# Kernel tuning notes

Hardware: AMD Instinct MI355X
Metric: run time of the kernel (lower is better)

## Reference

```python
import jax, jax.numpy as jnp
import numpy as np

# Dimensions: B batches, E links, T time steps, F flows, rank-r factors, K unrolled iters
B, E, T, F = 16, 256, 4096, 512
RANK = 10
NUM_ITER = 5


def setup_inputs() -> dict:
    key = jax.random.key(0)
    ks = jax.random.split(key, 9)
    Y = jax.random.normal(ks[0], (B, E, T), dtype=jnp.float32)
    R = (jax.random.uniform(ks[1], (B, E, F)) < 0.1).astype(jnp.float32)
    Omega = (jax.random.uniform(ks[2], (B, E, T)) < 0.9).astype(jnp.float32)
    P0 = jax.random.normal(ks[3], (B, E, RANK), dtype=jnp.float32) * 0.1
    Q0 = jax.random.normal(ks[4], (B, T, RANK), dtype=jnp.float32) * 0.1
    # per-iteration learned log-parameters of the unrolled network
    lam_log = jax.random.normal(ks[5], (NUM_ITER,), dtype=jnp.float32) * 0.1 - 1.0
    mu_log = jax.random.normal(ks[6], (NUM_ITER,), dtype=jnp.float32) * 0.1 - 1.0
    nu_log = jax.random.normal(ks[7], (NUM_ITER,), dtype=jnp.float32) * 0.1
    gamma_logit = jax.random.normal(ks[8], (NUM_ITER,), dtype=jnp.float32) * 0.1
    return {"Y": Y, "R": R, "Omega": Omega, "P0": P0, "Q0": Q0,
            "lam_log": lam_log, "mu_log": mu_log, "nu_log": nu_log,
            "gamma_logit": gamma_logit}


def reference(Y, R, Omega, P0, Q0, lam_log, mu_log, nu_log, gamma_logit):
    """Unrolled BSCA: Y ~ X + R @ A + noise on observed entries (Omega mask),
    X relaxed low-rank via factors P (B,E,r), Q (B,T,r); A sparse anomalies (B,F,T).
    Each iteration: rank-r ridge solves for P and Q (left=False -> rhs @ inv(lhs)),
    relaxed X update, soft-thresholded BSCA direction for A + convex-combination step."""
    rank = P0.shape[-1]
    eye = jnp.eye(rank, dtype=Y.dtype)
    X = Omega * Y                     # (B,E,T) init relaxed variable
    A = jnp.zeros((*Y.shape[:-2], R.shape[-1], Y.shape[-1]), dtype=Y.dtype)  # (B,F,T)
    P, Q = P0, Q0
    A_scale = (R * R).mT @ (Omega * Omega)          # (B,F,T)
    noobs = A_scale == 0
    A_scale_safe = A_scale + noobs.astype(Y.dtype)
    for k in range(NUM_ITER):
        lam = jnp.exp(lam_log[k])
        mu = jnp.exp(mu_log[k])
        nu = jnp.exp(nu_log[k])
        gamma = jax.nn.sigmoid(gamma_logit[k])
        regp = lam / nu
        # P update: P = (X @ Q) @ inv(Q^T Q + regp I)   (right solve; lhs symmetric)
        lhsQ = Q.mT @ Q + regp * eye                 # (B,r,r)
        P = jnp.linalg.solve(lhsQ, (X @ Q).mT).mT    # (B,E,r)
        # Q update: Q = (X^T @ P) @ inv(P^T P + regp I)
        lhsP = P.mT @ P + regp * eye
        Q = jnp.linalg.solve(lhsP, (X.mT @ P).mT).mT # (B,T,r)
        # X update (relaxed): X = (Omega*err + nu*P Q^T) / (Omega^2 + nu)
        RA = R @ A                                   # (B,E,T)
        err = Omega * (Y - RA)
        X = (Omega * err + nu * (P @ Q.mT)) / (Omega * Omega + nu)
        # A update: soft-thresholded best-response + convex combination step
        resid = Omega * (Y - X - RA)                 # (B,E,T)
        BA = A + (R.mT @ resid) / A_scale_safe       # (B,F,T)
        A_dir = jnp.sign(BA) * jnp.maximum(jnp.abs(BA) - mu / A_scale_safe, 0.0)
        A_dir = jnp.where(noobs, 0.0, A_dir)
        A = A + gamma * (A_dir - A)
    return A
```

## Files before the change

### kernel.cpp

```cpp
#include <hip/hip_runtime.h>
#include <stdint.h>

#define BB 16
#define EE 256
#define TT 4096
#define FF 512
#define RK 10
#define NIT 5

typedef short bf16x8 __attribute__((ext_vector_type(8)));
typedef float f32x4  __attribute__((ext_vector_type(4)));

__device__ __forceinline__ unsigned short f2bf(float x){
  unsigned int u = __float_as_uint(x);
  unsigned int r = (u + 0x7FFFu + ((u >> 16) & 1u)) >> 16;
  return (unsigned short)r;
}
__device__ __forceinline__ float bf2f(unsigned short s){
  return __uint_as_float(((unsigned int)s) << 16);
}

__device__ __forceinline__ void gld16(const void* g, void* l){
  __builtin_amdgcn_global_load_lds((const __attribute__((address_space(1))) unsigned int*)g,
                                   (__attribute__((address_space(3))) unsigned int*)l,
                                   16, 0, 0);
}

__device__ __forceinline__ int ssw(int r, int s){
  return ((s ^ (r & 3) ^ ((r >> 2) & 3)) << 3);
}


__global__ void k_params(const float* lam_log, const float* mu_log,
                         const float* nu_log, const float* gl, float* prm){
  int k = threadIdx.x;
  if (k < NIT){
    float lam = expf(lam_log[k]);
    float mu  = expf(mu_log[k]);
    float nu  = expf(nu_log[k]);
    float gam = 1.0f/(1.0f+expf(-gl[k]));
    prm[k*8+0]=lam; prm[k*8+1]=mu; prm[k*8+2]=nu; prm[k*8+3]=gam; prm[k*8+4]=lam/nu;
  }
}

__global__ void k_initX(const float4* __restrict__ Y, const float4* __restrict__ Om,
                        float4* __restrict__ X, ushort4* __restrict__ Omb){
  int i = blockIdx.x*256 + threadIdx.x;
  float4 y = Y[i], o = Om[i];
  X[i] = make_float4(y.x*o.x, y.y*o.y, y.z*o.z, y.w*o.w);
  ushort4 ob; ob.x=f2bf(o.x); ob.y=f2bf(o.y); ob.z=f2bf(o.z); ob.w=f2bf(o.w);
  Omb[i] = ob;
}

__global__ void k_ombit(const float* __restrict__ Om, unsigned int* __restrict__ Ombit){
  int tid = threadIdx.x;
  int wv = tid >> 6, lane = tid & 63;
  size_t base = (size_t)blockIdx.x*8192 + (size_t)wv*2048;
  for (int it=0; it<32; ++it){
    float om = Om[base + it*64 + lane];
    unsigned long long m = __ballot(om != 0.0f);
    if (lane==0)  Ombit[(base>>5) + it*2]     = (unsigned int)m;
    if (lane==32) Ombit[(base>>5) + it*2 + 1] = (unsigned int)(m>>32);
  }
}

__global__ void k_qtrans(const float* __restrict__ Q0, float* __restrict__ Qt){
  int idx = blockIdx.x*256 + threadIdx.x;
  int b = idx >> 12, t = idx & (TT-1);
  #pragma unroll
  for (int j=0;j<RK;j++)
    Qt[((size_t)b*RK + j)*TT + t] = Q0[(size_t)idx*RK + j];
}

__global__ void k_rbf(const float4* __restrict__ R, ushort4* __restrict__ Rb){
  int i = blockIdx.x*256 + threadIdx.x;
  float4 v = R[i];
  ushort4 o; o.x=f2bf(v.x); o.y=f2bf(v.y); o.z=f2bf(v.z); o.w=f2bf(v.w);
  Rb[i] = o;
}

__global__ void k_rtransb(const float* __restrict__ Rm, unsigned short* __restrict__ Rbt){
  int f = blockIdx.x, b = blockIdx.y, e = threadIdx.x;
  Rbt[((size_t)b*FF + f)*EE + e] = f2bf(Rm[((size_t)b*EE + e)*FF + f]);
}

__global__ void k_omtrans(const unsigned short* __restrict__ Omb,
                          unsigned short* __restrict__ OmbT){
  __shared__ unsigned short sT[64][66];
  int b  = blockIdx.z;
  int E0 = blockIdx.y*64, T0 = blockIdx.x*64;
  int tid = threadIdx.x;
  int fi = tid >> 4;
  int m  = tid & 15;
  #pragma unroll
  for (int pass=0; pass<4; ++pass){
    int e = pass*16 + fi;
    ushort4 v = *(const ushort4*)(Omb + ((size_t)(b*EE + E0 + e))*TT + T0 + m*4);
    sT[e][m*4+0]=v.x; sT[e][m*4+1]=v.y; sT[e][m*4+2]=v.z; sT[e][m*4+3]=v.w;
  }
  __syncthreads();
  #pragma unroll
  for (int pass=0; pass<4; ++pass){
    int t  = pass*16 + fi;
    int e4 = m*4;
    ushort4 o;
    o.x = sT[e4+0][t]; o.y = sT[e4+1][t];
    o.z = sT[e4+2][t]; o.w = sT[e4+3][t];
    *(ushort4*)(OmbT + ((size_t)b*TT + T0 + t)*EE + E0 + e4) = o;
  }
}


__global__ void k_lhsQ(const float* __restrict__ Qt, const float* __restrict__ prm,
                       float* __restrict__ lhs, int k){
  int p = blockIdx.x, b = blockIdx.y;
  int i = 0, rem = p;
  while (rem >= i+1){ rem -= (i+1); ++i; }
  int j = rem;
  const float* qi = Qt + ((size_t)b*RK + i)*TT;
  const float* qj = Qt + ((size_t)b*RK + j)*TT;
  float a = 0.0f;
  for (int t = threadIdx.x*4; t < TT; t += 1024){
    float4 x = *(const float4*)(qi+t);
    float4 y = *(const float4*)(qj+t);
    a += x.x*y.x + x.y*y.y + x.z*y.z + x.w*y.w;
  }
  __shared__ float red[256];
  red[threadIdx.x] = a; __syncthreads();
  for (int s=128; s>0; s>>=1){
    if (threadIdx.x < s) red[threadIdx.x] += red[threadIdx.x+s];
    __syncthreads();
  }
  if (threadIdx.x==0){
    float v = red[0];
    if (i==j) v += prm[k*8+4];
    lhs[(b*RK+i)*RK + j] = v;
    lhs[(b*RK+j)*RK + i] = v;
  }
}

__global__ void k_lhsP(const float* __restrict__ P, const float* __restrict__ prm,
                       float* __restrict__ lhs, int k){
  int p = blockIdx.x, b = blockIdx.y;
  int i = 0, rem = p;
  while (rem >= i+1){ rem -= (i+1); ++i; }
  int j = rem;
  int e = threadIdx.x;
  const float* pr = P + ((size_t)b*EE + e)*RK;
  float a = pr[i]*pr[j];
  __shared__ float red[256];
  red[threadIdx.x] = a; __syncthreads();
  for (int s=128; s>0; s>>=1){
    if (threadIdx.x < s) red[threadIdx.x] += red[threadIdx.x+s];
    __syncthreads();
  }
  if (threadIdx.x==0){
    float v = red[0];
    if (i==j) v += prm[k*8+4];
    lhs[(b*RK+i)*RK + j] = v;
    lhs[(b*RK+j)*RK + i] = v;
  }
}

__global__ void k_invert(const float* __restrict__ lhs, float* __restrict__ inv){
  int b = blockIdx.x;
  __shared__ float aug[RK][2*RK];
  int tid = threadIdx.x;
  int i = tid / (2*RK), j = tid % (2*RK);
  bool act = tid < RK*2*RK;
  if (act) aug[i][j] = (j < RK) ? lhs[(b*RK+i)*RK + j] : ((j-RK)==i ? 1.0f : 0.0f);
  __syncthreads();
  for (int kk=0; kk<RK; ++kk){
    float pinv = 1.0f / aug[kk][kk];
    __syncthreads();
    if (act && i==kk) aug[i][j] *= pinv;
    __syncthreads();
    float factor = (act && i!=kk) ? aug[i][kk] : 0.0f;
    float pivrow = act ? aug[kk][j] : 0.0f;
    __syncthreads();
    if (act && i!=kk) aug[i][j] -= factor * pivrow;
    __syncthreads();
  }
  if (act && j >= RK) inv[(b*RK+i)*RK + (j-RK)] = aug[i][j];
}

__global__ void k_Pupd(const float* __restrict__ X, const float* __restrict__ Qt,
                       const float* __restrict__ inv, float* __restrict__ P){
  int e = blockIdx.x, b = blockIdx.y;
  const float* xr = X + ((size_t)b*EE + e)*TT;
  const float* qb = Qt + (size_t)b*RK*TT;
  float acc[RK];
  #pragma unroll
  for (int j=0;j<RK;j++) acc[j]=0.0f;
  for (int t = threadIdx.x*4; t < TT; t += 1024){
    float4 x = *(const float4*)(xr+t);
    #pragma unroll
    for (int j=0;j<RK;j++){
      float4 q = *(const float4*)(qb + (size_t)j*TT + t);
      acc[j] += x.x*q.x + x.y*q.y + x.z*q.z + x.w*q.w;
    }
  }
  __shared__ float partial[4][RK];
  int lane = threadIdx.x & 63, wv = threadIdx.x >> 6;
  #pragma unroll
  for (int j=0;j<RK;j++){
    float v = acc[j];
    for (int s=32;s>0;s>>=1) v += __shfl_down(v, s, 64);
    if (lane==0) partial[wv][j] = v;
  }
  __syncthreads();
  if (threadIdx.x < RK){
    int i = threadIdx.x;
    float out = 0.0f;
    #pragma unroll
    for (int j=0;j<RK;j++){
      float xq = partial[0][j]+partial[1][j]+partial[2][j]+partial[3][j];
      out += xq * inv[(b*RK+j)*RK + i];
    }
    P[((size_t)b*EE + e)*RK + i] = out;
  }
}

__global__ void k_Qupd(const float* __restrict__ X, const float* __restrict__ P,
                       const float* __restrict__ inv, float* __restrict__ Qt){
  int b = blockIdx.y;
  int t = blockIdx.x*256 + threadIdx.x;
  __shared__ float sP[EE*RK];
  __shared__ float sInv[RK*RK];
  for (int i=threadIdx.x; i<EE*RK; i+=256) sP[i] = P[(size_t)b*EE*RK + i];
  if (threadIdx.x < RK*RK) sInv[threadIdx.x] = inv[b*RK*RK + threadIdx.x];
  __syncthreads();
  float acc[RK];
  #pragma unroll
  for (int j=0;j<RK;j++) acc[j]=0.0f;
  const float* xb = X + (size_t)b*EE*TT + t;
  for (int e=0;e<EE;e++){
    float x = xb[(size_t)e*TT];
    #pragma unroll
    for (int j=0;j<RK;j++) acc[j] += x * sP[e*RK+j];
  }
  #pragma unroll
  for (int i=0;i<RK;i++){
    float q = 0.0f;
    #pragma unroll
    for (int j=0;j<RK;j++) q += acc[j]*sInv[j*RK+i];
    Qt[((size_t)b*RK + i)*TT + t] = q;
  }
}

__global__ __launch_bounds__(256) void k_gemm1m(
    const unsigned short* __restrict__ Abt, const unsigned short* __restrict__ Rb,
    const float* __restrict__ Y, const unsigned int* __restrict__ Ombit,
    const float* __restrict__ Qt, const float* __restrict__ P,
    const float* __restrict__ prm, float* __restrict__ X,
    unsigned short* __restrict__ residT, int k)
{
  __shared__ __align__(16) unsigned char lds[20480];
  int id = blockIdx.x;
  int b  = id >> 7;
  int e0 = ((id >> 6) & 1) * 128;
  int t0 = (id & 63) * 64;
  int tid  = threadIdx.x;
  int lane = tid & 63, wid = tid >> 6;
  int lr = lane & 15, lg = lane >> 4;
  int wm = wid >> 1, wn = wid & 1;

  f32x4 acc[2][4];
  #pragma unroll
  for (int m=0;m<2;++m)
    #pragma unroll
    for (int n=0;n<4;++n)
      #pragma unroll
      for (int i=0;i<4;++i) acc[m][n][i]=0.0f;

  if (k > 0){
    int swz  = ((lg ^ (lr & 3) ^ ((lr >> 2) & 3)) << 4);
    int aoff = (wm*32 + lr)*64 + swz;
    int boff = 4096 + (wn*64 + lr)*64 + swz;
    int rA = tid >> 2, sA = tid & 3;
    int c0 = tid, c1 = tid + 256;
    int rB0 = c0 >> 2, sB0 = c0 & 3;
    int rB1 = c1 >> 2, sB1 = c1 & 3;
    const unsigned short* gA  = Abt + ((size_t)b*TT + t0 + rA)*FF + ssw(rA,sA);
    const unsigned short* gB0 = Rb  + ((size_t)(b*EE + e0 + rB0))*FF + ssw(rB0,sB0);
    const unsigned short* gB1 = Rb  + ((size_t)(b*EE + e0 + rB1))*FF + ssw(rB1,sB1);
    unsigned char* lA  = lds + tid*16;
    unsigned char* lB0 = lds + 4096 + c0*16;
    unsigned char* lB1 = lds + 4096 + c1*16;

    for (int kk=0; kk<16; ++kk){
      __syncthreads();
      int f0k = kk*32;
      gld16(gA  + f0k, lA);
      gld16(gB0 + f0k, lB0);
      gld16(gB1 + f0k, lB1);
      asm volatile("s_waitcnt vmcnt(0)" ::: "memory");
      __syncthreads();
      bf16x8 af[2], bb[4];
      #pragma unroll
      for (int m=0;m<2;++m) af[m] = *(const bf16x8*)(lds + aoff + m*1024);
      #pragma unroll
      for (int n=0;n<4;++n) bb[n] = *(const bf16x8*)(lds + boff + n*1024);
      #pragma unroll
      for (int m=0;m<2;++m)
        #pragma unroll
        for (int n=0;n<4;++n)
          acc[m][n] = __builtin_amdgcn_mfma_f32_16x16x32_bf16(af[m], bb[n], acc[m][n], 0, 0, 0);
    }
  }

  __syncthreads();
  unsigned short* wbuf = (unsigned short*)(lds + wid*2176);
  float* Pl = (float*)(lds + 12288);
  float* Ql = (float*)(lds + 12288 + 5120);
  for (int idx = tid; idx < 128*RK; idx += 256)
    Pl[idx] = P[((size_t)(b*EE + e0))*RK + idx];
  for (int idx = tid; idx < RK*64; idx += 256){
    int j = idx >> 6, t = idx & 63;
    Ql[idx] = Qt[((size_t)(b*RK + j))*TT + t0 + t];
  }
  __syncthreads();

  float nu = prm[k*8+2];
  #pragma unroll
  for (int m=0;m<2;++m){
    int tq = wm*32 + m*16 + lg*4;
    float4 ql4[RK];
    #pragma unroll
    for (int j=0;j<RK;++j) ql4[j] = *(const float4*)(Ql + j*64 + tq);
    asm volatile("" ::: "memory");
    #pragma unroll
    for (int n=0;n<4;++n){
      int eloc = wn*64 + n*16 + lr;
      const float* pr = Pl + eloc*RK;
      float4 pq = {0,0,0,0};
      #pragma unroll
      for (int j=0;j<RK;++j){
        float pj = pr[j];
        pq.x += pj*ql4[j].x; pq.y += pj*ql4[j].y;
        pq.z += pj*ql4[j].z; pq.w += pj*ql4[j].w;
      }
      f32x4 ra = acc[m][n];
      size_t off = ((size_t)(b*EE + e0 + eloc))*TT + t0 + tq;
      float4 y = *(const float4*)(Y + off);
      unsigned int w = Ombit[off >> 5];
      int sh = (int)(off & 31);
      float4 xo; float rs0, rs1, rs2, rs3;
      {
        float om2 = (w>>(sh+0))&1 ? 1.0f : 0.0f; float d = y.x - ra[0];
        xo.x = (om2*d + nu*pq.x)/(om2 + nu); rs0 = om2*(y.x - xo.x - ra[0]);
      }{
        float om2 = (w>>(sh+1))&1 ? 1.0f : 0.0f; float d = y.y - ra[1];
        xo.y = (om2*d + nu*pq.y)/(om2 + nu); rs1 = om2*(y.y - xo.y - ra[1]);
      }{
        float om2 = (w>>(sh+2))&1 ? 1.0f : 0.0f; float d = y.z - ra[2];
        xo.z = (om2*d + nu*pq.z)/(om2 + nu); rs2 = om2*(y.z - xo.z - ra[2]);
      }{
        float om2 = (w>>(sh+3))&1 ? 1.0f : 0.0f; float d = y.w - ra[3];
        xo.w = (om2*d + nu*pq.w)/(om2 + nu); rs3 = om2*(y.w - xo.w - ra[3]);
      }
      *(float4*)(X + off) = xo;
      int wc = n*16 + lr;
      wbuf[(lg*4+0)*68 + wc] = f2bf(rs0);
      wbuf[(lg*4+1)*68 + wc] = f2bf(rs1);
      wbuf[(lg*4+2)*68 + wc] = f2bf(rs2);
      wbuf[(lg*4+3)*68 + wc] = f2bf(rs3);
    }
    asm volatile("" ::: "memory");
    #pragma unroll
    for (int j2=0;j2<4;++j2){
      int row = j2*4 + lg;
      int c4  = lr*4;
      ushort4 vv = *(const ushort4*)(wbuf + row*68 + c4);
      *(ushort4*)(residT + ((size_t)b*TT + t0 + wm*32 + m*16 + row)*EE + e0 + wn*64 + c4) = vv;
    }
    asm volatile("" ::: "memory");
  }
}

__device__ __forceinline__ float aupd(float a, float g, unsigned short asu,
                                      float mu, float gamma){
  float as = bf2f(asu);
  bool no = (as == 0.0f);
  float rs = 1.0f / (no ? 1.0f : as);
  float ba = a + g*rs;
  float ad = copysignf(fmaxf(fabsf(ba) - mu*rs, 0.0f), ba);
  if (no) ad = 0.0f;
  return a + gamma*(ad - a);
}

__global__ __launch_bounds__(256) void k_gemm2m(
    const unsigned short* __restrict__ residT, const unsigned short* __restrict__ Rbt,
    const unsigned short* __restrict__ As, const float* __restrict__ prm,
    float* __restrict__ A, unsigned short* __restrict__ Abt, int k)
{
  __shared__ __align__(16) unsigned char lds[12288];
  int id = blockIdx.x;
  int b  = id >> 8;
  int f0 = ((id >> 5) & 7) * 64;
  int t0 = (id & 31) * 128;
  int tid  = threadIdx.x;
  int lane = tid & 63, wid = tid >> 6;
  int lr = lane & 15, lg = lane >> 4;
  int wm = wid >> 1, wn = wid & 1;

  f32x4 acc[4][2];
  #pragma unroll
  for (int m=0;m<4;++m)
    #pragma unroll
    for (int n=0;n<2;++n)
      #pragma unroll
      for (int i=0;i<4;++i) acc[m][n][i]=0.0f;

  int swz  = ((lg ^ (lr & 3) ^ ((lr >> 2) & 3)) << 4);
  int aoff = (wm*64 + lr)*64 + swz;
  int boff = 8192 + (wn*32 + lr)*64 + swz;
  int c0 = tid, c1 = tid + 256;
  int r0 = c0 >> 2, s0 = c0 & 3;
  int r1 = c1 >> 2, s1 = c1 & 3;
  int rB = tid >> 2, sB = tid & 3;
  const unsigned short* gA0 = residT + ((size_t)b*TT + t0 + r0)*EE + ssw(r0,s0);
  const unsigned short* gA1 = residT + ((size_t)b*TT + t0 + r1)*EE + ssw(r1,s1);
  const unsigned short* gB  = Rbt    + ((size_t)(b*FF + f0 + rB))*EE + ssw(rB,sB);
  unsigned char* lA0 = lds + c0*16;
  unsigned char* lA1 = lds + c1*16;
  unsigned char* lB  = lds + 8192 + tid*16;

  for (int kk=0; kk<8; ++kk){
    __syncthreads();
    int eoff = kk*32;
    gld16(gA0 + eoff, lA0);
    gld16(gA1 + eoff, lA1);
    gld16(gB  + eoff, lB);
    asm volatile("s_waitcnt vmcnt(0)" ::: "memory");
    __syncthreads();
    bf16x8 af[4], bb[2];
    #pragma unroll
    for (int m=0;m<4;++m) af[m] = *(const bf16x8*)(lds + aoff + m*1024);
    #pragma unroll
    for (int n=0;n<2;++n) bb[n] = *(const bf16x8*)(lds + boff + n*1024);
    #pragma unroll
    for (int m=0;m<4;++m)
      #pragma unroll
      for (int n=0;n<2;++n)
        acc[m][n] = __builtin_amdgcn_mfma_f32_16x16x32_bf16(af[m], bb[n], acc[m][n], 0, 0, 0);
  }

  __syncthreads();
  unsigned short* wbuf = (unsigned short*)(lds + wid*1152);
  float mu = prm[k*8+1], gamma = prm[k*8+3];
  bool emit = (k < NIT-1);
  #pragma unroll
  for (int m=0;m<4;++m){
    int tq = wm*64 + m*16 + lg*4;
    #pragma unroll
    for (int n=0;n<2;++n){
      int floc = wn*32 + n*16 + lr;
      size_t off = ((size_t)(b*FF + f0 + floc))*TT + t0 + tq;
      float4 a = *(const float4*)(A + off);
      ushort4 as4 = *(const ushort4*)(As + off);
      f32x4 g = acc[m][n];
      float4 an;
      an.x = aupd(a.x, g[0], as4.x, mu, gamma);
      an.y = aupd(a.y, g[1], as4.y, mu, gamma);
      an.z = aupd(a.z, g[2], as4.z, mu, gamma);
      an.w = aupd(a.w, g[3], as4.w, mu, gamma);
      *(float4*)(A + off) = an;
      if (emit){
        int wc = n*16 + lr;
        wbuf[(lg*4+0)*36 + wc] = f2bf(an.x);
        wbuf[(lg*4+1)*36 + wc] = f2bf(an.y);
        wbuf[(lg*4+2)*36 + wc] = f2bf(an.z);
        wbuf[(lg*4+3)*36 + wc] = f2bf(an.w);
      }
    }
    asm volatile("" ::: "memory");
    if (emit){
      #pragma unroll
      for (int j2=0;j2<2;++j2){
        int row = j2*8 + (lane >> 3);
        int c4  = (lane & 7)*4;
        ushort4 vv = *(const ushort4*)(wbuf + row*36 + c4);
        *(ushort4*)(Abt + ((size_t)b*TT + t0 + wm*64 + m*16 + row)*FF + f0 + wn*32 + c4) = vv;
      }
    }
    asm volatile("" ::: "memory");
  }
}

__global__ __launch_bounds__(256) void k_ascalem(
    const unsigned short* __restrict__ OmbT, const unsigned short* __restrict__ Rbt,
    unsigned short* __restrict__ As)
{
  __shared__ __align__(16) unsigned char lds[16384];
  int id = blockIdx.x;
  int b  = id >> 7;
  int f0 = ((id >> 5) & 3) * 128;
  int t0 = (id & 31) * 128;
  int tid  = threadIdx.x;
  int lane = tid & 63, wid = tid >> 6;
  int lr = lane & 15, lg = lane >> 4;
  int wm = wid >> 1, wn = wid & 1;

  f32x4 acc[4][4];
  #pragma unroll
  for (int m=0;m<4;++m)
    #pragma unroll
    for (int n=0;n<4;++n)
      #pragma unroll
      for (int i=0;i<4;++i) acc[m][n][i]=0.0f;

  int swz  = ((lg ^ (lr & 3) ^ ((lr >> 2) & 3)) << 4);
  int aoff = (wm*64 + lr)*64 + swz;
  int boff = 8192 + (wn*64 + lr)*64 + swz;
  int c0 = tid, c1 = tid + 256;
  int r0 = c0 >> 2, s0 = c0 & 3;
  int r1 = c1 >> 2, s1 = c1 & 3;
  const unsigned short* gA0 = OmbT + ((size_t)b*TT + t0 + r0)*EE + ssw(r0,s0);
  const unsigned short* gA1 = OmbT + ((size_t)b*TT + t0 + r1)*EE + ssw(r1,s1);
  const unsigned short* gB0 = Rbt  + ((size_t)(b*FF + f0 + r0))*EE + ssw(r0,s0);
  const unsigned short* gB1 = Rbt  + ((size_t)(b*FF + f0 + r1))*EE + ssw(r1,s1);
  unsigned char* lA0 = lds + c0*16;
  unsigned char* lA1 = lds + c1*16;
  unsigned char* lB0 = lds + 8192 + c0*16;
  unsigned char* lB1 = lds + 8192 + c1*16;

  for (int kk=0; kk<8; ++kk){
    __syncthreads();
    int eoff = kk*32;
    gld16(gA0 + eoff, lA0);
    gld16(gA1 + eoff, lA1);
    gld16(gB0 + eoff, lB0);
    gld16(gB1 + eoff, lB1);
    asm volatile("s_waitcnt vmcnt(0)" ::: "memory");
    __syncthreads();
    bf16x8 af[4], bb[4];
    #pragma unroll
    for (int m=0;m<4;++m) af[m] = *(const bf16x8*)(lds + aoff + m*1024);
    #pragma unroll
    for (int n=0;n<4;++n) bb[n] = *(const bf16x8*)(lds + boff + n*1024);
    #pragma unroll
    for (int m=0;m<4;++m)
      #pragma unroll
      for (int n=0;n<4;++n)
        acc[m][n] = __builtin_amdgcn_mfma_f32_16x16x32_bf16(af[m], bb[n], acc[m][n], 0, 0, 0);
  }

  #pragma unroll
  for (int m=0;m<4;++m){
    int tq = wm*64 + m*16 + lg*4;
    #pragma unroll
    for (int n=0;n<4;++n){
      int floc = wn*64 + n*16 + lr;
      size_t off = ((size_t)(b*FF + f0 + floc))*TT + t0 + tq;
      ushort4 o;
      o.x = f2bf(acc[m][n][0]); o.y = f2bf(acc[m][n][1]);
      o.z = f2bf(acc[m][n][2]); o.w = f2bf(acc[m][n][3]);
      *(ushort4*)(As + off) = o;
    }
  }
}


extern "C" void kernel_launch(void* const* d_in, const int* in_sizes, int n_in,
                              void* d_out, int out_size, void* d_ws, size_t ws_size,
                              hipStream_t stream){
  const float* Y   = (const float*)d_in[0];
  const float* Rm  = (const float*)d_in[1];
  const float* Om  = (const float*)d_in[2];
  const float* P0  = (const float*)d_in[3];
  const float* Q0  = (const float*)d_in[4];
  const float* lam = (const float*)d_in[5];
  const float* mu  = (const float*)d_in[6];
  const float* nu  = (const float*)d_in[7];
  const float* gl  = (const float*)d_in[8];
  float* A = (float*)d_out;

  char* ws = (char*)d_ws;
  const size_t X_OFF    = 0;
  const size_t REST_OFF = X_OFF    + (size_t)BB*EE*TT*4;
  const size_t OMB_OFF  = REST_OFF + (size_t)BB*TT*EE*2;
  const size_t AS_OFF   = OMB_OFF  + (size_t)BB*EE*TT*2;
  const size_t QT_OFF   = AS_OFF   + (size_t)BB*FF*TT*2;
  const size_t P_OFF    = QT_OFF   + (size_t)BB*RK*TT*4;
  const size_t LHS_OFF  = P_OFF    + (size_t)BB*EE*RK*4;
  const size_t INV_OFF  = LHS_OFF  + (size_t)BB*RK*RK*4;
  const size_t PRM_OFF  = INV_OFF  + (size_t)BB*RK*RK*4;
  const size_t RB_OFF   = PRM_OFF  + 4096;
  const size_t RBT_OFF  = RB_OFF   + (size_t)BB*EE*FF*2;
  const size_t OMBT_OFF = RBT_OFF  + (size_t)BB*FF*EE*2;
  const size_t ABT_OFF  = OMBT_OFF + (size_t)BB*TT*EE*2;
  const size_t OBIT_OFF = ABT_OFF  + (size_t)BB*TT*FF*2;

  float* X    = (float*)(ws + X_OFF);
  unsigned short* residT = (unsigned short*)(ws + REST_OFF);
  unsigned short* Omb    = (unsigned short*)(ws + OMB_OFF);
  unsigned short* As     = (unsigned short*)(ws + AS_OFF);
  float* Qt   = (float*)(ws + QT_OFF);
  float* P    = (float*)(ws + P_OFF);
  float* lhs  = (float*)(ws + LHS_OFF);
  float* inv  = (float*)(ws + INV_OFF);
  float* prm  = (float*)(ws + PRM_OFF);
  unsigned short* Rb    = (unsigned short*)(ws + RB_OFF);
  unsigned short* Rbt   = (unsigned short*)(ws + RBT_OFF);
  unsigned short* OmbT  = (unsigned short*)(ws + OMBT_OFF);
  unsigned short* Abt   = (unsigned short*)(ws + ABT_OFF);
  unsigned int*   Ombit = (unsigned int*)(ws + OBIT_OFF);

  (void)P0; (void)in_sizes; (void)n_in; (void)ws_size;

  hipMemsetAsync(d_out, 0, (size_t)out_size*sizeof(float), stream);
  k_params<<<1, 64, 0, stream>>>(lam, mu, nu, gl, prm);
  k_initX<<<BB*EE*TT/4/256, 256, 0, stream>>>((const float4*)Y, (const float4*)Om,
                                              (float4*)X, (ushort4*)Omb);
  k_ombit<<<BB*EE*TT/8192, 256, 0, stream>>>(Om, Ombit);
  k_qtrans<<<BB*TT/256, 256, 0, stream>>>(Q0, Qt);
  k_rbf<<<BB*EE*FF/4/256, 256, 0, stream>>>((const float4*)Rm, (ushort4*)Rb);
  k_rtransb<<<dim3(FF, BB), 256, 0, stream>>>(Rm, Rbt);
  k_omtrans<<<dim3(TT/64, EE/64, BB), 256, 0, stream>>>(Omb, OmbT);
  k_ascalem<<<2048, 256, 0, stream>>>(OmbT, Rbt, As);

  for (int k=0; k<NIT; ++k){
    k_lhsQ  <<<dim3(55, BB), 256, 0, stream>>>(Qt, prm, lhs, k);
    k_invert<<<BB, 256, 0, stream>>>(lhs, inv);
    k_Pupd  <<<dim3(EE, BB), 256, 0, stream>>>(X, Qt, inv, P);
    k_lhsP  <<<dim3(55, BB), 256, 0, stream>>>(P, prm, lhs, k);
    k_invert<<<BB, 256, 0, stream>>>(lhs, inv);
    k_Qupd  <<<dim3(TT/256, BB), 256, 0, stream>>>(X, P, inv, Qt);
    k_gemm1m<<<2048, 256, 0, stream>>>(Abt, Rb, Y, Ombit, Qt, P, prm, X, residT, k);
    k_gemm2m<<<4096, 256, 0, stream>>>(residT, Rbt, As, prm, A, Abt, k);
  }
}
```

Before: 1.806 ms.

## Store X and A iterates in bf16 and drop redundant fp32 traffic

After: 1.786 ms. About the same (-1.1%).

```diff
diff --git a/kernel.cpp b/kernel.cpp
--- a/kernel.cpp
+++ b/kernel.cpp
@@ -44,12 +44,11 @@
 }
 
 __global__ void k_initX(const float4* __restrict__ Y, const float4* __restrict__ Om,
-                        float4* __restrict__ X, ushort4* __restrict__ Omb){
+                        ushort4* __restrict__ Xb){
   int i = blockIdx.x*256 + threadIdx.x;
   float4 y = Y[i], o = Om[i];
-  X[i] = make_float4(y.x*o.x, y.y*o.y, y.z*o.z, y.w*o.w);
-  ushort4 ob; ob.x=f2bf(o.x); ob.y=f2bf(o.y); ob.z=f2bf(o.z); ob.w=f2bf(o.w);
-  Omb[i] = ob;
+  ushort4 xb; xb.x=f2bf(y.x*o.x); xb.y=f2bf(y.y*o.y); xb.z=f2bf(y.z*o.z); xb.w=f2bf(y.w*o.w);
+  Xb[i] = xb;
 }
 
 __global__ void k_ombit(const float* __restrict__ Om, unsigned int* __restrict__ Ombit){
@@ -84,7 +83,7 @@
   Rbt[((size_t)b*FF + f)*EE + e] = f2bf(Rm[((size_t)b*EE + e)*FF + f]);
 }
 
-__global__ void k_omtrans(const unsigned short* __restrict__ Omb,
+__global__ void k_omtrans(const float* __restrict__ Om,
                           unsigned short* __restrict__ OmbT){
   __shared__ unsigned short sT[64][66];
   int b  = blockIdx.z;
@@ -95,8 +94,9 @@
   #pragma unroll
   for (int pass=0; pass<4; ++pass){
     int e = pass*16 + fi;
-    ushort4 v = *(const ushort4*)(Omb + ((size_t)(b*EE + E0 + e))*TT + T0 + m*4);
-    sT[e][m*4+0]=v.x; sT[e][m*4+1]=v.y; sT[e][m*4+2]=v.z; sT[e][m*4+3]=v.w;
+    float4 v = *(const float4*)(Om + ((size_t)(b*EE + E0 + e))*TT + T0 + m*4);
+    sT[e][m*4+0]=f2bf(v.x); sT[e][m*4+1]=f2bf(v.y);
+    sT[e][m*4+2]=f2bf(v.z); sT[e][m*4+3]=f2bf(v.w);
   }
   __syncthreads();
   #pragma unroll
@@ -184,20 +184,25 @@
   if (act && j >= RK) inv[(b*RK+i)*RK + (j-RK)] = aug[i][j];
 }
 
-__global__ void k_Pupd(const float* __restrict__ X, const float* __restrict__ Qt,
+__global__ void k_Pupd(const unsigned short* __restrict__ Xb, const float* __restrict__ Qt,
                        const float* __restrict__ inv, float* __restrict__ P){
   int e = blockIdx.x, b = blockIdx.y;
-  const float* xr = X + ((size_t)b*EE + e)*TT;
+  const unsigned short* xr = Xb + ((size_t)b*EE + e)*TT;
   const float* qb = Qt + (size_t)b*RK*TT;
   float acc[RK];
   #pragma unroll
   for (int j=0;j<RK;j++) acc[j]=0.0f;
-  for (int t = threadIdx.x*4; t < TT; t += 1024){
-    float4 x = *(const float4*)(xr+t);
+  for (int t = threadIdx.x*8; t < TT; t += 2048){
+    bf16x8 xv = *(const bf16x8*)(xr+t);
+    float xf[8];
+    #pragma unroll
+    for (int i=0;i<8;++i) xf[i] = bf2f((unsigned short)xv[i]);
     #pragma unroll
     for (int j=0;j<RK;j++){
-      float4 q = *(const float4*)(qb + (size_t)j*TT + t);
-      acc[j] += x.x*q.x + x.y*q.y + x.z*q.z + x.w*q.w;
+      float4 qa = *(const float4*)(qb + (size_t)j*TT + t);
+      float4 qc = *(const float4*)(qb + (size_t)j*TT + t + 4);
+      acc[j] += xf[0]*qa.x + xf[1]*qa.y + xf[2]*qa.z + xf[3]*qa.w
+              + xf[4]*qc.x + xf[5]*qc.y + xf[6]*qc.z + xf[7]*qc.w;
     }
   }
   __shared__ float partial[4][RK];
@@ -221,7 +226,7 @@
   }
 }
 
-__global__ void k_Qupd(const float* __restrict__ X, const float* __restrict__ P,
+__global__ void k_Qupd(const unsigned short* __restrict__ Xb, const float* __restrict__ P,
                        const float* __restrict__ inv, float* __restrict__ Qt){
   int b = blockIdx.y;
   int t = blockIdx.x*256 + threadIdx.x;
@@ -233,9 +238,9 @@
   float acc[RK];
   #pragma unroll
   for (int j=0;j<RK;j++) acc[j]=0.0f;
-  const float* xb = X + (size_t)b*EE*TT + t;
+  const unsigned short* xb = Xb + (size_t)b*EE*TT + t;
   for (int e=0;e<EE;e++){
-    float x = xb[(size_t)e*TT];
+    float x = bf2f(xb[(size_t)e*TT]);
     #pragma unroll
     for (int j=0;j<RK;j++) acc[j] += x * sP[e*RK+j];
   }
@@ -252,7 +257,7 @@
     const unsigned short* __restrict__ Abt, const unsigned short* __restrict__ Rb,
     const float* __restrict__ Y, const unsigned int* __restrict__ Ombit,
     const float* __restrict__ Qt, const float* __restrict__ P,
-    const float* __restrict__ prm, float* __restrict__ X,
+    const float* __restrict__ prm, unsigned short* __restrict__ Xb,
     unsigned short* __restrict__ residT, int k)
 {
   __shared__ __align__(16) unsigned char lds[20480];
@@ -322,6 +327,7 @@
   __syncthreads();
 
   float nu = prm[k*8+2];
+  bool wx = (k < NIT-1);
   #pragma unroll
   for (int m=0;m<2;++m){
     int tq = wm*32 + m*16 + lg*4;
@@ -345,21 +351,21 @@
       float4 y = *(const float4*)(Y + off);
       unsigned int w = Ombit[off >> 5];
       int sh = (int)(off & 31);
-      float4 xo; float rs0, rs1, rs2, rs3;
+      float rs0, rs1, rs2, rs3; ushort4 xb4;
       {
         float om2 = (w>>(sh+0))&1 ? 1.0f : 0.0f; float d = y.x - ra[0];
-        xo.x = (om2*d + nu*pq.x)/(om2 + nu); rs0 = om2*(y.x - xo.x - ra[0]);
+        float x = (om2*d + nu*pq.x)/(om2 + nu); rs0 = om2*(y.x - x - ra[0]); xb4.x = f2bf(x);
       }{
         float om2 = (w>>(sh+1))&1 ? 1.0f : 0.0f; float d = y.y - ra[1];
-        xo.y = (om2*d + nu*pq.y)/(om2 + nu); rs1 = om2*(y.y - xo.y - ra[1]);
+        float x = (om2*d + nu*pq.y)/(om2 + nu); rs1 = om2*(y.y - x - ra[1]); xb4.y = f2bf(x);
       }{
         float om2 = (w>>(sh+2))&1 ? 1.0f : 0.0f; float d = y.z - ra[2];
-        xo.z = (om2*d + nu*pq.z)/(om2 + nu); rs2 = om2*(y.z - xo.z - ra[2]);
+        float x = (om2*d + nu*pq.z)/(om2 + nu); rs2 = om2*(y.z - x - ra[2]); xb4.z = f2bf(x);
       }{
         float om2 = (w>>(sh+3))&1 ? 1.0f : 0.0f; float d = y.w - ra[3];
-        xo.w = (om2*d + nu*pq.w)/(om2 + nu); rs3 = om2*(y.w - xo.w - ra[3]);
+        float x = (om2*d + nu*pq.w)/(om2 + nu); rs3 = om2*(y.w - x - ra[3]); xb4.w = f2bf(x);
       }
-      *(float4*)(X + off) = xo;
+      if (wx) *(ushort4*)(Xb + off) = xb4;
       int wc = n*16 + lr;
       wbuf[(lg*4+0)*68 + wc] = f2bf(rs0);
       wbuf[(lg*4+1)*68 + wc] = f2bf(rs1);
@@ -392,7 +398,8 @@
 __global__ __launch_bounds__(256) void k_gemm2m(
     const unsigned short* __restrict__ residT, const unsigned short* __restrict__ Rbt,
     const unsigned short* __restrict__ As, const float* __restrict__ prm,
-    float* __restrict__ A, unsigned short* __restrict__ Abt, int k)
+    unsigned short* __restrict__ Abf, unsigned short* __restrict__ Abt,
+    float* __restrict__ Afin, int k)
 {
   __shared__ __align__(16) unsigned char lds[12288];
   int id = blockIdx.x;
@@ -457,7 +464,13 @@
     for (int n=0;n<2;++n){
       int floc = wn*32 + n*16 + lr;
       size_t off = ((size_t)(b*FF + f0 + floc))*TT + t0 + tq;
-      float4 a = *(const float4*)(A + off);
+      float4 a;
+      if (k > 0){
+        ushort4 ab4 = *(const ushort4*)(Abf + off);
+        a.x = bf2f(ab4.x); a.y = bf2f(ab4.y); a.z = bf2f(ab4.z); a.w = bf2f(ab4.w);
+      } else {
+        a = make_float4(0.f, 0.f, 0.f, 0.f);
+      }
       ushort4 as4 = *(const ushort4*)(As + off);
       f32x4 g = acc[m][n];
       float4 an;
@@ -465,13 +478,17 @@
       an.y = aupd(a.y, g[1], as4.y, mu, gamma);
       an.z = aupd(a.z, g[2], as4.z, mu, gamma);
       an.w = aupd(a.w, g[3], as4.w, mu, gamma);
-      *(float4*)(A + off) = an;
       if (emit){
+        ushort4 ab;
+        ab.x = f2bf(an.x); ab.y = f2bf(an.y); ab.z = f2bf(an.z); ab.w = f2bf(an.w);
+        *(ushort4*)(Abf + off) = ab;
         int wc = n*16 + lr;
-        wbuf[(lg*4+0)*36 + wc] = f2bf(an.x);
-        wbuf[(lg*4+1)*36 + wc] = f2bf(an.y);
-        wbuf[(lg*4+2)*36 + wc] = f2bf(an.z);
-        wbuf[(lg*4+3)*36 + wc] = f2bf(an.w);
+        wbuf[(lg*4+0)*36 + wc] = ab.x;
+        wbuf[(lg*4+1)*36 + wc] = ab.y;
+        wbuf[(lg*4+2)*36 + wc] = ab.z;
+        wbuf[(lg*4+3)*36 + wc] = ab.w;
+      } else {
+        *(float4*)(Afin + off) = an;
       }
     }
     asm volatile("" ::: "memory");
@@ -577,10 +594,9 @@
   float* A = (float*)d_out;
 
   char* ws = (char*)d_ws;
-  const size_t X_OFF    = 0;
-  const size_t REST_OFF = X_OFF    + (size_t)BB*EE*TT*4;
-  const size_t OMB_OFF  = REST_OFF + (size_t)BB*TT*EE*2;
-  const size_t AS_OFF   = OMB_OFF  + (size_t)BB*EE*TT*2;
+  const size_t XB_OFF   = 0;
+  const size_t REST_OFF = XB_OFF   + (size_t)BB*EE*TT*2;
+  const size_t AS_OFF   = REST_OFF + (size_t)BB*TT*EE*2;
   const size_t QT_OFF   = AS_OFF   + (size_t)BB*FF*TT*2;
   const size_t P_OFF    = QT_OFF   + (size_t)BB*RK*TT*4;
   const size_t LHS_OFF  = P_OFF    + (size_t)BB*EE*RK*4;
@@ -591,10 +607,10 @@
   const size_t OMBT_OFF = RBT_OFF  + (size_t)BB*FF*EE*2;
   const size_t ABT_OFF  = OMBT_OFF + (size_t)BB*TT*EE*2;
   const size_t OBIT_OFF = ABT_OFF  + (size_t)BB*TT*FF*2;
-
-  float* X    = (float*)(ws + X_OFF);
+  const size_t ABF_OFF  = OBIT_OFF + (size_t)BB*EE*TT/8;
+
+  unsigned short* Xb     = (unsigned short*)(ws + XB_OFF);
   unsigned short* residT = (unsigned short*)(ws + REST_OFF);
-  unsigned short* Omb    = (unsigned short*)(ws + OMB_OFF);
   unsigned short* As     = (unsigned short*)(ws + AS_OFF);
   float* Qt   = (float*)(ws + QT_OFF);
   float* P    = (float*)(ws + P_OFF);
@@ -606,28 +622,28 @@
   unsigned short* OmbT  = (unsigned short*)(ws + OMBT_OFF);
   unsigned short* Abt   = (unsigned short*)(ws + ABT_OFF);
   unsigned int*   Ombit = (unsigned int*)(ws + OBIT_OFF);
-
-  (void)P0; (void)in_sizes; (void)n_in; (void)ws_size;
-
-  hipMemsetAsync(d_out, 0, (size_t)out_size*sizeof(float), stream);
+  unsigned short* Abf   = (unsigned short*)(ws + ABF_OFF);
+
+  (void)P0; (void)in_sizes; (void)n_in; (void)ws_size; (void)out_size;
+
   k_params<<<1, 64, 0, stream>>>(lam, mu, nu, gl, prm);
   k_initX<<<BB*EE*TT/4/256, 256, 0, stream>>>((const float4*)Y, (const float4*)Om,
-                                              (float4*)X, (ushort4*)Omb);
+                                              (ushort4*)Xb);
   k_ombit<<<BB*EE*TT/8192, 256, 0, stream>>>(Om, Ombit);
   k_qtrans<<<BB*TT/256, 256, 0, stream>>>(Q0, Qt);
   k_rbf<<<BB*EE*FF/4/256, 256, 0, stream>>>((const float4*)Rm, (ushort4*)Rb);
   k_rtransb<<<dim3(FF, BB), 256, 0, stream>>>(Rm, Rbt);
-  k_omtrans<<<dim3(TT/64, EE/64, BB), 256, 0, stream>>>(Omb, OmbT);
+  k_omtrans<<<dim3(TT/64, EE/64, BB), 256, 0, stream>>>(Om, OmbT);
   k_ascalem<<<2048, 256, 0, stream>>>(OmbT, Rbt, As);
 
   for (int k=0; k<NIT; ++k){
     k_lhsQ  <<<dim3(55, BB), 256, 0, stream>>>(Qt, prm, lhs, k);
     k_invert<<<BB, 256, 0, stream>>>(lhs, inv);
-    k_Pupd  <<<dim3(EE, BB), 256, 0, stream>>>(X, Qt, inv, P);
+    k_Pupd  <<<dim3(EE, BB), 256, 0, stream>>>(Xb, Qt, inv, P);
     k_lhsP  <<<dim3(55, BB), 256, 0, stream>>>(P, prm, lhs, k);
     k_invert<<<BB, 256, 0, stream>>>(lhs, inv);
-    k_Qupd  <<<dim3(TT/256, BB), 256, 0, stream>>>(X, P, inv, Qt);
-    k_gemm1m<<<2048, 256, 0, stream>>>(Abt, Rb, Y, Ombit, Qt, P, prm, X, residT, k);
-    k_gemm2m<<<4096, 256, 0, stream>>>(residT, Rbt, As, prm, A, Abt, k);
-  }
-}
+    k_Qupd  <<<dim3(TT/256, BB), 256, 0, stream>>>(Xb, P, inv, Qt);
+    k_gemm1m<<<2048, 256, 0, stream>>>(Abt, Rb, Y, Ombit, Qt, P, prm, Xb, residT, k);
+    k_gemm2m<<<4096, 256, 0, stream>>>(residT, Rbt, As, prm, Abf, Abt, A, k);
+  }
+}
```
